# Kernel tuning notes

Hardware: AMD Instinct MI355X
Metric: run time of the kernel (lower is better)

The kernel has to match this reference:

```python
import jax, jax.numpy as jnp
import numpy as np

N = 100000   # nodes
E = 1600000  # edges
IN = 768     # in_dim
H = 128      # hidden_dim
G = 64       # graphs per batch


def setup_inputs() -> dict:
    key = jax.random.key(0)
    ks = jax.random.split(key, 9)
    x = jax.random.normal(ks[0], (N, IN), jnp.float32)
    edge_index = jax.random.randint(ks[1], (2, E), 0, N, dtype=jnp.int64)
    batch = jnp.sort(jax.random.randint(ks[2], (N,), 0, G, dtype=jnp.int64))
    W1 = jax.random.normal(ks[3], (IN, H), jnp.float32) / np.float32(np.sqrt(IN))
    b1 = jax.random.normal(ks[4], (H,), jnp.float32) * 0.01
    W2 = jax.random.normal(ks[5], (H, H), jnp.float32) / np.float32(np.sqrt(H))
    b2 = jax.random.normal(ks[6], (H,), jnp.float32) * 0.01
    Wh = jax.random.normal(ks[7], (H, 2), jnp.float32) / np.float32(np.sqrt(H))
    bh = jax.random.normal(ks[8], (2,), jnp.float32) * 0.01
    return dict(x=x, edge_index=edge_index, batch=batch, W1=W1, b1=b1,
                W2=W2, b2=b2, Wh=Wh, bh=bh, num_graphs=G)


def gcn_conv(x, src, dst, W, b, n):
    # PyG GCNConv default: add self-loops (already in src/dst), symmetric norm.
    deg = jax.ops.segment_sum(jnp.ones_like(dst, x.dtype), dst, num_segments=n)
    dis = jnp.where(deg > 0, jax.lax.rsqrt(deg), jnp.zeros_like(deg))
    h = x @ W                                   # [n, out]
    norm = (dis[src] * dis[dst])[:, None]       # [E+n, 1]
    out = jax.ops.segment_sum(h[src] * norm, dst, num_segments=n)
    return out + b


def reference(x, edge_index, batch, W1, b1, W2, b2, Wh, bh, num_graphs):
    n = x.shape[0]
    loop = jnp.arange(n, dtype=edge_index.dtype)
    src = jnp.concatenate([edge_index[0], loop])
    dst = jnp.concatenate([edge_index[1], loop])
    h = jax.nn.relu(gcn_conv(x, src, dst, W1, b1, n))   # dropout = eval identity
    h = jax.nn.relu(gcn_conv(h, src, dst, W2, b2, n))
    summed = jax.ops.segment_sum(h, batch, num_segments=num_graphs)
    counts = jax.ops.segment_sum(jnp.ones((n, 1), h.dtype), batch, num_segments=num_graphs)
    emb = summed / jnp.maximum(counts, 1.0)             # global_mean_pool
    return emb @ Wh + bh
```

## Files before the change

### kernel.cpp

```cpp
#include <hip/hip_runtime.h>
#include <hip/hip_bf16.h>
#include <hip/hip_fp16.h>

static constexpr int N_NODES  = 100000;
static constexpr int N_EDGES  = 1600000;
static constexpr int DIM_IN   = 768;
static constexpr int DIM_H    = 128;
static constexpr int N_GRAPHS = 64;
static constexpr int NB_SCAN  = (N_NODES + 255) / 256;

typedef __attribute__((ext_vector_type(8))) _Float16 half8;
typedef __attribute__((ext_vector_type(4))) float f32x4;

__global__ void k_indeg(const int* __restrict__ edst, int* __restrict__ indeg) {
    int e = blockIdx.x * 256 + threadIdx.x;
    if (e < N_EDGES) atomicAdd(&indeg[edst[e]], 1);
}

__global__ void k_convW(const float* __restrict__ W1, const float* __restrict__ W2,
                        _Float16* __restrict__ W1t, _Float16* __restrict__ W2t) {
    int i = blockIdx.x * 256 + threadIdx.x;
    const int total1 = DIM_IN * DIM_H;
    if (i < total1) {
        int k = i >> 7, n = i & 127;
        W1t[(size_t)n * DIM_IN + k] = (_Float16)W1[i];
    } else if (i < total1 + DIM_H * DIM_H) {
        int j = i - total1;
        int k = j >> 7, n = j & 127;
        W2t[(size_t)n * DIM_H + k] = (_Float16)W2[j];
    }
}

__global__ void k_scan1(const int* __restrict__ indeg, int* __restrict__ rp,
                        int* __restrict__ bsum, float* __restrict__ dis) {
    __shared__ int s[256];
    int t = threadIdx.x;
    int i = blockIdx.x * 256 + t;
    int v = (i < N_NODES) ? indeg[i] : 0;
    s[t] = v;
    __syncthreads();
    for (int off = 1; off < 256; off <<= 1) {
        int x = (t >= off) ? s[t - off] : 0;
        __syncthreads();
        s[t] += x;
        __syncthreads();
    }
    if (i < N_NODES) {
        rp[i] = s[t] - v;
        dis[i] = rsqrtf((float)v + 1.0f);
    }
    if (t == 255) bsum[blockIdx.x] = s[255];
}

__global__ void k_scan2(int* __restrict__ bsum, const int* __restrict__ batch,
                        int* __restrict__ gstart) {
    __shared__ int s[512];
    int t = threadIdx.x;
    int v = (t < NB_SCAN) ? bsum[t] : 0;
    s[t] = v;
    __syncthreads();
    for (int off = 1; off < 512; off <<= 1) {
        int x = (t >= off) ? s[t - off] : 0;
        __syncthreads();
        s[t] += x;
        __syncthreads();
    }
    if (t < NB_SCAN) bsum[t] = s[t] - v;
    if (t <= N_GRAPHS) {
        int lo = 0, hi = N_NODES;
        while (lo < hi) {
            int mid = (lo + hi) >> 1;
            if (batch[mid] < t) lo = mid + 1; else hi = mid;
        }
        gstart[t] = lo;
    }
}

#define BKV 64
#define LDSTR 72

template<int K, bool AFP32, bool FUSE_SCATTER>
__global__ __launch_bounds__(256) void k_gemm_mfma(const void* __restrict__ Av,
                                                   const _Float16* __restrict__ Wt,
                                                   _Float16* __restrict__ C,
                                                   int nrows,
                                                   const int* __restrict__ esrc,
                                                   const int* __restrict__ edst,
                                                   const int* __restrict__ rp,
                                                   const int* __restrict__ bsum,
                                                   const float* __restrict__ dis,
                                                   int* __restrict__ cursor,
                                                   uint2* __restrict__ csrw,
                                                   int gemm_blocks) {
    __shared__ ushort As[64 * LDSTR];
    __shared__ ushort Bs[128 * LDSTR];

    if (FUSE_SCATTER && (int)blockIdx.x >= gemm_blocks) {
        int e = (blockIdx.x - gemm_blocks) * 256 + threadIdx.x;
        if (e < N_EDGES) {
            int d = edst[e];
            int sv = esrc[e];
            int pos = atomicAdd(&cursor[d], 1);
            uint2 val;
            val.x = (uint)sv;
            val.y = __float_as_uint(dis[sv]);
            csrw[rp[d] + bsum[d >> 8] + pos] = val;
        }
        return;
    }

    const int t = threadIdx.x;
    const int row0 = blockIdx.x * 64;
    const int sa_row = t >> 2;
    const int sa_col = (t & 3) * 16;
    const int sw_row = t >> 1;
    const int sw_col = (t & 1) * 32;
    const int l = t & 63;
    const int wv = t >> 6;
    const int wm = wv >> 1, wn = wv & 1;
    const int lr = l & 15;
    const int lk8 = (l >> 4) * 8;
    const bool arow_ok = (row0 + sa_row < nrows);

    f32x4 acc[2][4];
    const f32x4 zero = {0.f, 0.f, 0.f, 0.f};
    #pragma unroll
    for (int m = 0; m < 2; ++m)
        #pragma unroll
        for (int n = 0; n < 4; ++n) acc[m][n] = zero;

    for (int k0 = 0; k0 < K; k0 += BKV) {
        if (AFP32) {
            union { _Float16 h[16]; uint4 q[2]; } cv;
            float f[16];
            if (arow_ok) {
                const float4* Ap = (const float4*)((const float*)Av +
                    (size_t)(row0 + sa_row) * K + k0 + sa_col);
                #pragma unroll
                for (int i = 0; i < 4; ++i) *(float4*)&f[4 * i] = Ap[i];
            } else {
                #pragma unroll
                for (int i = 0; i < 16; ++i) f[i] = 0.f;
            }
            #pragma unroll
            for (int i = 0; i < 16; ++i) cv.h[i] = (_Float16)f[i];
            *(uint4*)&As[sa_row * LDSTR + sa_col]     = cv.q[0];
            *(uint4*)&As[sa_row * LDSTR + sa_col + 8] = cv.q[1];
        } else {
            uint4 q0 = {0, 0, 0, 0}, q1 = {0, 0, 0, 0};
            if (arow_ok) {
                const uint4* Ap = (const uint4*)((const _Float16*)Av +
                    (size_t)(row0 + sa_row) * K + k0 + sa_col);
                q0 = Ap[0]; q1 = Ap[1];
            }
            *(uint4*)&As[sa_row * LDSTR + sa_col]     = q0;
            *(uint4*)&As[sa_row * LDSTR + sa_col + 8] = q1;
        }
        {
            const uint4* Wp = (const uint4*)(Wt + (size_t)sw_row * K + k0 + sw_col);
            uint4 w0 = Wp[0], w1 = Wp[1], w2 = Wp[2], w3 = Wp[3];
            *(uint4*)&Bs[sw_row * LDSTR + sw_col + 0]  = w0;
            *(uint4*)&Bs[sw_row * LDSTR + sw_col + 8]  = w1;
            *(uint4*)&Bs[sw_row * LDSTR + sw_col + 16] = w2;
            *(uint4*)&Bs[sw_row * LDSTR + sw_col + 24] = w3;
        }
        __syncthreads();

        #pragma unroll
        for (int ks2 = 0; ks2 < 2; ++ks2) {
            half8 a[2], b[4];
            #pragma unroll
            for (int m = 0; m < 2; ++m)
                a[m] = *(const half8*)&As[(wm * 32 + m * 16 + lr) * LDSTR + ks2 * 32 + lk8];
            #pragma unroll
            for (int n = 0; n < 4; ++n)
                b[n] = *(const half8*)&Bs[(wn * 64 + n * 16 + lr) * LDSTR + ks2 * 32 + lk8];
            #pragma unroll
            for (int m = 0; m < 2; ++m)
                #pragma unroll
                for (int n = 0; n < 4; ++n)
                    acc[m][n] = __builtin_amdgcn_mfma_f32_16x16x32_f16(a[m], b[n], acc[m][n], 0, 0, 0);
        }
        __syncthreads();
    }

    #pragma unroll
    for (int m = 0; m < 2; ++m) {
        #pragma unroll
        for (int n = 0; n < 4; ++n) {
            int col = wn * 64 + n * 16 + lr;
            #pragma unroll
            for (int j = 0; j < 4; ++j) {
                int row = row0 + wm * 32 + m * 16 + (l >> 4) * 4 + j;
                if (row < nrows)
                    C[(size_t)row * DIM_H + col] = (_Float16)acc[m][n][j];
            }
        }
    }
}

__device__ __forceinline__ void acc8(uint4 u, float w, float* a) {
    __half2 h0 = *(__half2*)&u.x;
    __half2 h1 = *(__half2*)&u.y;
    __half2 h2 = *(__half2*)&u.z;
    __half2 h3 = *(__half2*)&u.w;
    a[0] += __low2float(h0) * w; a[1] += __high2float(h0) * w;
    a[2] += __low2float(h1) * w; a[3] += __high2float(h1) * w;
    a[4] += __low2float(h2) * w; a[5] += __high2float(h2) * w;
    a[6] += __low2float(h3) * w; a[7] += __high2float(h3) * w;
}

__global__ __launch_bounds__(256) void k_agg(const _Float16* __restrict__ hin,
                                             const uint2* __restrict__ csrw,
                                             const int* __restrict__ rp,
                                             const int* __restrict__ bsum,
                                             const int* __restrict__ indeg,
                                             const float* __restrict__ dis,
                                             const float* __restrict__ bias,
                                             _Float16* __restrict__ hout) {
    int node = (blockIdx.x * 256 + threadIdx.x) >> 6;
    int lane = threadIdx.x & 63;
    if (node >= N_NODES) return;
    int q  = lane >> 4;
    int cl = lane & 15;
    float di = dis[node];
    int beg = rp[node] + bsum[node >> 8];
    int cnt = indeg[node];

    float a[8] = {0.f, 0.f, 0.f, 0.f, 0.f, 0.f, 0.f, 0.f};

    {
        uint s; float w;
        if (q == 0)             { s = (uint)node; w = di * di; }
        else if (q - 1 < cnt)   { uint2 p = csrw[beg + q - 1]; s = p.x; w = __uint_as_float(p.y) * di; }
        else                    { s = (uint)node; w = 0.f; }
        uint4 u = ((const uint4*)(hin + (size_t)s * DIM_H))[cl];
        acc8(u, w, a);
    }
    const uint2* cp = csrw + beg + 3;
    int m = cnt - 3;
    int i = 0;
    for (; i + 8 <= m; i += 8) {
        uint2 p0 = cp[i + q];
        uint2 p1 = cp[i + 4 + q];
        float w0 = __uint_as_float(p0.y) * di;
        float w1 = __uint_as_float(p1.y) * di;
        uint4 u0 = ((const uint4*)(hin + (size_t)p0.x * DIM_H))[cl];
        uint4 u1 = ((const uint4*)(hin + (size_t)p1.x * DIM_H))[cl];
        acc8(u0, w0, a);
        acc8(u1, w1, a);
    }
    for (; i < m; i += 4) {
        int idx = i + q;
        uint s; float w;
        if (idx < m) { uint2 p = cp[idx]; s = p.x; w = __uint_as_float(p.y) * di; }
        else         { s = (uint)node;    w = 0.f; }
        uint4 u = ((const uint4*)(hin + (size_t)s * DIM_H))[cl];
        acc8(u, w, a);
    }

    #pragma unroll
    for (int j = 0; j < 8; ++j) {
        a[j] += __shfl_xor(a[j], 16);
        a[j] += __shfl_xor(a[j], 32);
    }

    if (q == 0) {
        float4 b0 = ((const float4*)bias)[cl * 2];
        float4 b1 = ((const float4*)bias)[cl * 2 + 1];
        __half2 h0 = __floats2half2_rn(fmaxf(a[0] + b0.x, 0.f), fmaxf(a[1] + b0.y, 0.f));
        __half2 h1 = __floats2half2_rn(fmaxf(a[2] + b0.z, 0.f), fmaxf(a[3] + b0.w, 0.f));
        __half2 h2 = __floats2half2_rn(fmaxf(a[4] + b1.x, 0.f), fmaxf(a[5] + b1.y, 0.f));
        __half2 h3 = __floats2half2_rn(fmaxf(a[6] + b1.z, 0.f), fmaxf(a[7] + b1.w, 0.f));
        uint4 o;
        o.x = *(uint*)&h0; o.y = *(uint*)&h1; o.z = *(uint*)&h2; o.w = *(uint*)&h3;
        ((uint4*)(hout + (size_t)node * DIM_H))[cl] = o;
    }
}

#define PSPLIT 8
__global__ __launch_bounds__(256) void k_pool(const _Float16* __restrict__ h,
                                              const int* __restrict__ gstart,
                                              float* __restrict__ pooled2) {
    int g  = blockIdx.x >> 3;
    int sp = blockIdx.x & 7;
    int r0 = gstart[g], r1 = gstart[g + 1];
    int count = r1 - r0;
    int chunk = (count + PSPLIT - 1) / PSPLIT;
    int aS = r0 + sp * chunk;
    int bE = min(aS + chunk, r1);
    int c  = threadIdx.x & 63;
    int rr = threadIdx.x >> 6;
    float s0a = 0.f, s1a = 0.f, s0b = 0.f, s1b = 0.f;
    int r = aS + rr;
    for (; r + 4 < bE; r += 8) {
        uint ua = ((const uint*)(h + (size_t)r * DIM_H))[c];
        uint ub = ((const uint*)(h + (size_t)(r + 4) * DIM_H))[c];
        __half2 ha = *(__half2*)&ua;
        __half2 hb = *(__half2*)&ub;
        s0a += __low2float(ha); s1a += __high2float(ha);
        s0b += __low2float(hb); s1b += __high2float(hb);
    }
    if (r < bE) {
        uint ua = ((const uint*)(h + (size_t)r * DIM_H))[c];
        __half2 ha = *(__half2*)&ua;
        s0a += __low2float(ha); s1a += __high2float(ha);
    }
    float s0 = s0a + s0b, s1 = s1a + s1b;
    __shared__ float sm0[4][64], sm1[4][64];
    sm0[rr][c] = s0; sm1[rr][c] = s1;
    __syncthreads();
    if (rr == 0) {
        float v0 = sm0[0][c] + sm0[1][c] + sm0[2][c] + sm0[3][c];
        float v1 = sm1[0][c] + sm1[1][c] + sm1[2][c] + sm1[3][c];
        float* dst = pooled2 + (size_t)(g * PSPLIT + sp) * DIM_H;
        dst[2 * c]     = v0;
        dst[2 * c + 1] = v1;
    }
}

__global__ __launch_bounds__(128) void k_head(const float* __restrict__ pooled2,
                                              const int* __restrict__ gstart,
                                              const float* __restrict__ Wh,
                                              const float* __restrict__ bh,
                                              float* __restrict__ out) {
    int g = blockIdx.x;
    int c = threadIdx.x;
    float s = 0.f;
    #pragma unroll
    for (int sp = 0; sp < PSPLIT; ++sp)
        s += pooled2[(size_t)(g * PSPLIT + sp) * DIM_H + c];
    float cntg = (float)(gstart[g + 1] - gstart[g]);
    float e = s / fmaxf(cntg, 1.0f);
    __shared__ float s0[128], s1[128];
    s0[c] = e * Wh[c * 2 + 0];
    s1[c] = e * Wh[c * 2 + 1];
    __syncthreads();
    for (int off = 64; off > 0; off >>= 1) {
        if (c < off) { s0[c] += s0[c + off]; s1[c] += s1[c + off]; }
        __syncthreads();
    }
    if (c == 0) {
        out[g * 2 + 0] = s0[0] + bh[0];
        out[g * 2 + 1] = s1[0] + bh[1];
    }
}

extern "C" void kernel_launch(void* const* d_in, const int* in_sizes, int n_in,
                              void* d_out, int out_size, void* d_ws, size_t ws_size,
                              hipStream_t stream) {
    const float* x    = (const float*)d_in[0];
    const int*   esrc = (const int*)d_in[1];
    const int*   edst = esrc + N_EDGES;
    const int*   batch= (const int*)d_in[2];
    const float* W1   = (const float*)d_in[3];
    const float* b1   = (const float*)d_in[4];
    const float* W2   = (const float*)d_in[5];
    const float* b2   = (const float*)d_in[6];
    const float* Wh   = (const float*)d_in[7];
    const float* bh   = (const float*)d_in[8];
    float* out = (float*)d_out;

    char* ws = (char*)d_ws;
    size_t off = 0;
    auto alloc = [&](size_t bytes) {
        void* p = ws + off;
        off += (bytes + 255) & ~(size_t)255;
        return p;
    };
    _Float16* bufZ   = (_Float16*)alloc((size_t)N_NODES * DIM_H * 2);
    _Float16* bufH   = (_Float16*)alloc((size_t)N_NODES * DIM_H * 2);
    float*    dis    = (float*)alloc((size_t)N_NODES * 4);
    int*      deg2   = (int*)  alloc((size_t)2 * N_NODES * 4);
    int*      indeg  = deg2;
    int*      cursor = deg2 + N_NODES;
    int*      rp     = (int*)  alloc((size_t)N_NODES * 4);
    uint2*    csrw   = (uint2*)alloc((size_t)N_EDGES * 8);
    int*      bsum   = (int*)  alloc(512 * 4);
    float*    pooled2= (float*)alloc((size_t)N_GRAPHS * PSPLIT * DIM_H * 4);
    int*      gstart = (int*)  alloc((N_GRAPHS + 1) * 4);
    _Float16* W1t    = (_Float16*)alloc((size_t)DIM_IN * DIM_H * 2);
    _Float16* W2t    = (_Float16*)alloc((size_t)DIM_H * DIM_H * 2);

    hipMemsetAsync(deg2, 0, (size_t)2 * N_NODES * 4, stream);

    int convblocks = (DIM_IN * DIM_H + DIM_H * DIM_H + 255) / 256;
    k_convW  <<<convblocks, 256, 0, stream>>>(W1, W2, W1t, W2t);

    k_indeg  <<<(N_EDGES + 255) / 256, 256, 0, stream>>>(edst, indeg);
    k_scan1  <<<NB_SCAN, 256, 0, stream>>>(indeg, rp, bsum, dis);
    k_scan2  <<<1, 512, 0, stream>>>(bsum, batch, gstart);

    int gblocks = (N_NODES + 63) / 64;
    int scblocks = (N_EDGES + 255) / 256;
    k_gemm_mfma<DIM_IN, true, true><<<gblocks + scblocks, 256, 0, stream>>>(
        x, W1t, bufZ, N_NODES, esrc, edst, rp, bsum, dis, cursor, csrw, gblocks);
    k_agg<<<(N_NODES + 3) / 4, 256, 0, stream>>>(bufZ, csrw, rp, bsum, indeg, dis, b1, bufH);
    k_gemm_mfma<DIM_H, false, false><<<gblocks, 256, 0, stream>>>(
        bufH, W2t, bufZ, N_NODES, nullptr, nullptr, nullptr, nullptr, nullptr, nullptr, nullptr, gblocks);
    k_agg<<<(N_NODES + 3) / 4, 256, 0, stream>>>(bufZ, csrw, rp, bsum, indeg, dis, b2, bufH);

    k_pool<<<N_GRAPHS * PSPLIT, 256, 0, stream>>>(bufH, gstart, pooled2);
    k_head<<<N_GRAPHS, 128, 0, stream>>>(pooled2, gstart, Wh, bh, out);
}
```

Before: 395.2 us.

## Double-buffer GEMM tiles via direct global-to-LDS loads with swizzled layout

Replaces the register-staged GEMM tile loads with global_load_lds async copies into double-buffered shared memory, so the next K-tile loads while the MFMAs run on the current one. The fp32 A tile is stored raw in LDS with an XOR swizzle and converted to fp16 at fragment-read time. The K step drops from 64 to 32, and row bounds are handled by clamping the row index. Explicit vmcnt waits and raw barriers manage the pipeline, which depends on exact counting of outstanding loads.

```diff
diff --git a/kernel.cpp b/kernel.cpp
--- a/kernel.cpp
+++ b/kernel.cpp
@@ -11,6 +11,12 @@
 
 typedef __attribute__((ext_vector_type(8))) _Float16 half8;
 typedef __attribute__((ext_vector_type(4))) float f32x4;
+
+__device__ __forceinline__ void gld16(const void* g, void* l) {
+    __builtin_amdgcn_global_load_lds(
+        (const __attribute__((address_space(1))) void*)g,
+        (__attribute__((address_space(3))) void*)l, 16, 0, 0);
+}
 
 __global__ void k_indeg(const int* __restrict__ edst, int* __restrict__ indeg) {
     int e = blockIdx.x * 256 + threadIdx.x;
@@ -76,8 +82,7 @@
     }
 }
 
-#define BKV 64
-#define LDSTR 72
+#define BKQ 32
 
 template<int K, bool AFP32, bool FUSE_SCATTER>
 __global__ __launch_bounds__(256) void k_gemm_mfma(const void* __restrict__ Av,
@@ -92,8 +97,8 @@
                                                    int* __restrict__ cursor,
                                                    uint2* __restrict__ csrw,
                                                    int gemm_blocks) {
-    __shared__ ushort As[64 * LDSTR];
-    __shared__ ushort Bs[128 * LDSTR];
+    __shared__ uint Asb[2][2048];
+    __shared__ uint Wsb[2][2048];
 
     if (FUSE_SCATTER && (int)blockIdx.x >= gemm_blocks) {
         int e = (blockIdx.x - gemm_blocks) * 256 + threadIdx.x;
@@ -111,16 +116,42 @@
 
     const int t = threadIdx.x;
     const int row0 = blockIdx.x * 64;
-    const int sa_row = t >> 2;
-    const int sa_col = (t & 3) * 16;
-    const int sw_row = t >> 1;
-    const int sw_col = (t & 1) * 32;
     const int l = t & 63;
     const int wv = t >> 6;
     const int wm = wv >> 1, wn = wv & 1;
     const int lr = l & 15;
     const int lk8 = (l >> 4) * 8;
-    const bool arow_ok = (row0 + sa_row < nrows);
+    constexpr int NT = K / BKQ;
+
+    auto stage = [&](int b, int k0) {
+        if (AFP32) {
+            #pragma unroll
+            for (int j = 0; j < 2; ++j) {
+                int c = 2 * wv + j;
+                int row = c * 8 + (l >> 3);
+                int grow = min(row0 + row, nrows - 1);
+                int dkb = (l & 7) * 4;
+                int sdk = dkb ^ ((row & 7) << 2);
+                const float* gp = (const float*)Av + (size_t)grow * K + k0 + sdk;
+                gld16(gp, &Asb[b][c * 256]);
+            }
+        } else {
+            int c = wv;
+            int row = c * 16 + (l >> 2);
+            int grow = min(row0 + row, nrows - 1);
+            int dwb = (l & 3) * 4;
+            const _Float16* gp = (const _Float16*)Av + (size_t)grow * K + k0 + dwb * 2;
+            gld16(gp, &Asb[b][c * 256]);
+        }
+        #pragma unroll
+        for (int j = 0; j < 2; ++j) {
+            int c = 2 * wv + j;
+            int n = c * 16 + (l >> 2);
+            int dwb = (l & 3) * 4;
+            const _Float16* gp = Wt + (size_t)n * K + k0 + dwb * 2;
+            gld16(gp, &Wsb[b][c * 256]);
+        }
+    };
 
     f32x4 acc[2][4];
     const f32x4 zero = {0.f, 0.f, 0.f, 0.f};
@@ -129,59 +160,54 @@
         #pragma unroll
         for (int n = 0; n < 4; ++n) acc[m][n] = zero;
 
-    for (int k0 = 0; k0 < K; k0 += BKV) {
-        if (AFP32) {
-            union { _Float16 h[16]; uint4 q[2]; } cv;
-            float f[16];
-            if (arow_ok) {
-                const float4* Ap = (const float4*)((const float*)Av +
-                    (size_t)(row0 + sa_row) * K + k0 + sa_col);
-                #pragma unroll
-                for (int i = 0; i < 4; ++i) *(float4*)&f[4 * i] = Ap[i];
+    stage(0, 0);
+    for (int tt = 0; tt < NT; ++tt) {
+        const int bb = tt & 1;
+        if (tt + 1 < NT) {
+            stage(bb ^ 1, (tt + 1) * BKQ);
+            if constexpr (AFP32) asm volatile("s_waitcnt vmcnt(4)" ::: "memory");
+            else                 asm volatile("s_waitcnt vmcnt(3)" ::: "memory");
+        } else {
+            asm volatile("s_waitcnt vmcnt(0)" ::: "memory");
+        }
+        __builtin_amdgcn_s_barrier();
+        asm volatile("" ::: "memory");
+
+        half8 af[2];
+        #pragma unroll
+        for (int m = 0; m < 2; ++m) {
+            int row_l = wm * 32 + m * 16 + lr;
+            if (AFP32) {
+                int x = (row_l & 7) << 2;
+                const uint* base = &Asb[bb][row_l * 32];
+                float4 f0 = *(const float4*)&base[lk8 ^ x];
+                float4 f1 = *(const float4*)&base[(lk8 + 4) ^ x];
+                half8 r;
+                r[0] = (_Float16)f0.x; r[1] = (_Float16)f0.y;
+                r[2] = (_Float16)f0.z; r[3] = (_Float16)f0.w;
+                r[4] = (_Float16)f1.x; r[5] = (_Float16)f1.y;
+                r[6] = (_Float16)f1.z; r[7] = (_Float16)f1.w;
+                af[m] = r;
             } else {
-                #pragma unroll
-                for (int i = 0; i < 16; ++i) f[i] = 0.f;
+                const ushort* base = (const ushort*)&Asb[bb][0];
+                af[m] = *(const half8*)&base[row_l * 32 + lk8];
             }
-            #pragma unroll
-            for (int i = 0; i < 16; ++i) cv.h[i] = (_Float16)f[i];
-            *(uint4*)&As[sa_row * LDSTR + sa_col]     = cv.q[0];
-            *(uint4*)&As[sa_row * LDSTR + sa_col + 8] = cv.q[1];
-        } else {
-            uint4 q0 = {0, 0, 0, 0}, q1 = {0, 0, 0, 0};
-            if (arow_ok) {
-                const uint4* Ap = (const uint4*)((const _Float16*)Av +
-                    (size_t)(row0 + sa_row) * K + k0 + sa_col);
-                q0 = Ap[0]; q1 = Ap[1];
-            }
-            *(uint4*)&As[sa_row * LDSTR + sa_col]     = q0;
-            *(uint4*)&As[sa_row * LDSTR + sa_col + 8] = q1;
-        }
-        {
-            const uint4* Wp = (const uint4*)(Wt + (size_t)sw_row * K + k0 + sw_col);
-            uint4 w0 = Wp[0], w1 = Wp[1], w2 = Wp[2], w3 = Wp[3];
-            *(uint4*)&Bs[sw_row * LDSTR + sw_col + 0]  = w0;
-            *(uint4*)&Bs[sw_row * LDSTR + sw_col + 8]  = w1;
-            *(uint4*)&Bs[sw_row * LDSTR + sw_col + 16] = w2;
-            *(uint4*)&Bs[sw_row * LDSTR + sw_col + 24] = w3;
-        }
-        __syncthreads();
-
-        #pragma unroll
-        for (int ks2 = 0; ks2 < 2; ++ks2) {
-            half8 a[2], b[4];
-            #pragma unroll
-            for (int m = 0; m < 2; ++m)
-                a[m] = *(const half8*)&As[(wm * 32 + m * 16 + lr) * LDSTR + ks2 * 32 + lk8];
+        }
+        half8 wf[4];
+        #pragma unroll
+        for (int n = 0; n < 4; ++n) {
+            int nn = wn * 64 + n * 16 + lr;
+            const ushort* base = (const ushort*)&Wsb[bb][0];
+            wf[n] = *(const half8*)&base[nn * 32 + lk8];
+        }
+        #pragma unroll
+        for (int m = 0; m < 2; ++m)
             #pragma unroll
             for (int n = 0; n < 4; ++n)
-                b[n] = *(const half8*)&Bs[(wn * 64 + n * 16 + lr) * LDSTR + ks2 * 32 + lk8];
-            #pragma unroll
-            for (int m = 0; m < 2; ++m)
-                #pragma unroll
-                for (int n = 0; n < 4; ++n)
-                    acc[m][n] = __builtin_amdgcn_mfma_f32_16x16x32_f16(a[m], b[n], acc[m][n], 0, 0, 0);
-        }
-        __syncthreads();
+                acc[m][n] = __builtin_amdgcn_mfma_f32_16x16x32_f16(af[m], wf[n], acc[m][n], 0, 0, 0);
+
+        asm volatile("" ::: "memory");
+        __builtin_amdgcn_s_barrier();
     }
 
     #pragma unroll
```

New measurement: 408.5 us. 3.4% more time.

## Fuse in-degree counting into first GEMM and scatter CSR in separate kernel

Applied to the files above, without the earlier changes.

Moves the in-degree atomic counting into extra blocks of the first GEMM launch, so it overlaps with the x@W1 matmul. The CSR scatter that was previously fused there now runs as its own kernel after the scan. A fixup kernel precomputes global row pointers and initial cursors so the scatter and aggregation kernels no longer add the block offsets themselves. This trades one overlap for another: the degree pass is overlapped instead of the heavier scatter, and the scatter becomes a serial kernel, so the net effect depends on which one costs more.

```diff
diff --git a/kernel.cpp b/kernel.cpp
--- a/kernel.cpp
+++ b/kernel.cpp
@@ -11,11 +11,6 @@
 
 typedef __attribute__((ext_vector_type(8))) _Float16 half8;
 typedef __attribute__((ext_vector_type(4))) float f32x4;
-
-__global__ void k_indeg(const int* __restrict__ edst, int* __restrict__ indeg) {
-    int e = blockIdx.x * 256 + threadIdx.x;
-    if (e < N_EDGES) atomicAdd(&indeg[edst[e]], 1);
-}
 
 __global__ void k_convW(const float* __restrict__ W1, const float* __restrict__ W2,
                         _Float16* __restrict__ W1t, _Float16* __restrict__ W2t) {
@@ -76,36 +71,47 @@
     }
 }
 
+__global__ void k_fixup(const int* __restrict__ rp, const int* __restrict__ bsum,
+                        int* __restrict__ rpg, int* __restrict__ cursor2) {
+    int i = blockIdx.x * 256 + threadIdx.x;
+    if (i < N_NODES) {
+        int v = rp[i] + bsum[i >> 8];
+        rpg[i] = v;
+        cursor2[i] = v;
+    }
+}
+
+__global__ void k_scatter(const int* __restrict__ esrc, const int* __restrict__ edst,
+                          const float* __restrict__ dis,
+                          int* __restrict__ cursor2, uint2* __restrict__ csrw) {
+    int e = blockIdx.x * 256 + threadIdx.x;
+    if (e >= N_EDGES) return;
+    int d = edst[e];
+    int sv = esrc[e];
+    int pos = atomicAdd(&cursor2[d], 1);
+    uint2 val;
+    val.x = (uint)sv;
+    val.y = __float_as_uint(dis[sv]);
+    csrw[pos] = val;
+}
+
 #define BKV 64
 #define LDSTR 72
 
-template<int K, bool AFP32, bool FUSE_SCATTER>
+template<int K, bool AFP32, bool FUSE_INDEG>
 __global__ __launch_bounds__(256) void k_gemm_mfma(const void* __restrict__ Av,
                                                    const _Float16* __restrict__ Wt,
                                                    _Float16* __restrict__ C,
                                                    int nrows,
-                                                   const int* __restrict__ esrc,
                                                    const int* __restrict__ edst,
-                                                   const int* __restrict__ rp,
-                                                   const int* __restrict__ bsum,
-                                                   const float* __restrict__ dis,
-                                                   int* __restrict__ cursor,
-                                                   uint2* __restrict__ csrw,
+                                                   int* __restrict__ indeg,
                                                    int gemm_blocks) {
     __shared__ ushort As[64 * LDSTR];
     __shared__ ushort Bs[128 * LDSTR];
 
-    if (FUSE_SCATTER && (int)blockIdx.x >= gemm_blocks) {
+    if (FUSE_INDEG && (int)blockIdx.x >= gemm_blocks) {
         int e = (blockIdx.x - gemm_blocks) * 256 + threadIdx.x;
-        if (e < N_EDGES) {
-            int d = edst[e];
-            int sv = esrc[e];
-            int pos = atomicAdd(&cursor[d], 1);
-            uint2 val;
-            val.x = (uint)sv;
-            val.y = __float_as_uint(dis[sv]);
-            csrw[rp[d] + bsum[d >> 8] + pos] = val;
-        }
+        if (e < N_EDGES) atomicAdd(&indeg[edst[e]], 1);
         return;
     }
 
@@ -212,8 +218,7 @@
 
 __global__ __launch_bounds__(256) void k_agg(const _Float16* __restrict__ hin,
                                              const uint2* __restrict__ csrw,
-                                             const int* __restrict__ rp,
-                                             const int* __restrict__ bsum,
+                                             const int* __restrict__ rpg,
                                              const int* __restrict__ indeg,
                                              const float* __restrict__ dis,
                                              const float* __restrict__ bias,
@@ -224,7 +229,7 @@
     int q  = lane >> 4;
     int cl = lane & 15;
     float di = dis[node];
-    int beg = rp[node] + bsum[node >> 8];
+    int beg = rpg[node];
     int cnt = indeg[node];
 
     float a[8] = {0.f, 0.f, 0.f, 0.f, 0.f, 0.f, 0.f, 0.f};
@@ -371,10 +376,10 @@
     _Float16* bufZ   = (_Float16*)alloc((size_t)N_NODES * DIM_H * 2);
     _Float16* bufH   = (_Float16*)alloc((size_t)N_NODES * DIM_H * 2);
     float*    dis    = (float*)alloc((size_t)N_NODES * 4);
-    int*      deg2   = (int*)  alloc((size_t)2 * N_NODES * 4);
-    int*      indeg  = deg2;
-    int*      cursor = deg2 + N_NODES;
+    int*      indeg  = (int*)  alloc((size_t)N_NODES * 4);
     int*      rp     = (int*)  alloc((size_t)N_NODES * 4);
+    int*      rpg    = (int*)  alloc((size_t)N_NODES * 4);
+    int*      cursor2= (int*)  alloc((size_t)N_NODES * 4);
     uint2*    csrw   = (uint2*)alloc((size_t)N_EDGES * 8);
     int*      bsum   = (int*)  alloc(512 * 4);
     float*    pooled2= (float*)alloc((size_t)N_GRAPHS * PSPLIT * DIM_H * 4);
@@ -382,23 +387,24 @@
     _Float16* W1t    = (_Float16*)alloc((size_t)DIM_IN * DIM_H * 2);
     _Float16* W2t    = (_Float16*)alloc((size_t)DIM_H * DIM_H * 2);
 
-    hipMemsetAsync(deg2, 0, (size_t)2 * N_NODES * 4, stream);
+    hipMemsetAsync(indeg, 0, (size_t)N_NODES * 4, stream);
 
     int convblocks = (DIM_IN * DIM_H + DIM_H * DIM_H + 255) / 256;
     k_convW  <<<convblocks, 256, 0, stream>>>(W1, W2, W1t, W2t);
 
-    k_indeg  <<<(N_EDGES + 255) / 256, 256, 0, stream>>>(edst, indeg);
+    int gblocks = (N_NODES + 63) / 64;
+    int eblocks = (N_EDGES + 255) / 256;
+    k_gemm_mfma<DIM_IN, true, true><<<gblocks + eblocks, 256, 0, stream>>>(
+        x, W1t, bufZ, N_NODES, edst, indeg, gblocks);
     k_scan1  <<<NB_SCAN, 256, 0, stream>>>(indeg, rp, bsum, dis);
     k_scan2  <<<1, 512, 0, stream>>>(bsum, batch, gstart);
-
-    int gblocks = (N_NODES + 63) / 64;
-    int scblocks = (N_EDGES + 255) / 256;
-    k_gemm_mfma<DIM_IN, true, true><<<gblocks + scblocks, 256, 0, stream>>>(
-        x, W1t, bufZ, N_NODES, esrc, edst, rp, bsum, dis, cursor, csrw, gblocks);
-    k_agg<<<(N_NODES + 3) / 4, 256, 0, stream>>>(bufZ, csrw, rp, bsum, indeg, dis, b1, bufH);
+    k_fixup  <<<NB_SCAN, 256, 0, stream>>>(rp, bsum, rpg, cursor2);
+    k_scatter<<<eblocks, 256, 0, stream>>>(esrc, edst, dis, cursor2, csrw);
+
+    k_agg<<<(N_NODES + 3) / 4, 256, 0, stream>>>(bufZ, csrw, rpg, indeg, dis, b1, bufH);
     k_gemm_mfma<DIM_H, false, false><<<gblocks, 256, 0, stream>>>(
-        bufH, W2t, bufZ, N_NODES, nullptr, nullptr, nullptr, nullptr, nullptr, nullptr, nullptr, gblocks);
-    k_agg<<<(N_NODES + 3) / 4, 256, 0, stream>>>(bufZ, csrw, rp, bsum, indeg, dis, b2, bufH);
+        bufH, W2t, bufZ, N_NODES, nullptr, nullptr, gblocks);
+    k_agg<<<(N_NODES + 3) / 4, 256, 0, stream>>>(bufZ, csrw, rpg, indeg, dis, b2, bufH);
 
     k_pool<<<N_GRAPHS * PSPLIT, 256, 0, stream>>>(bufH, gstart, pooled2);
     k_head<<<N_GRAPHS, 128, 0, stream>>>(pooled2, gstart, Wh, bh, out);
```

Measured after the change: 386.6 us (median of 2 runs). 2.2% less time.
